# Optimization experiments

Measured on AMD Instinct MI355X. Metric: run time of the kernel, lower is better.

The kernel has to match this reference:

```python
import jax, jax.numpy as jnp
import numpy as np

TOP_K = 8
TEMPERATURE = 0.07
EPS = 1e-12  # matches torch F.normalize eps


def l2norm(x):
    return x / jnp.maximum(jnp.linalg.norm(x, axis=-1, keepdims=True), EPS)


def setup_inputs() -> dict:
    key = jax.random.key(0)
    k1, k2, k3, k4 = jax.random.split(key, 4)
    B, D, V, U, Q = 256, 768, 50257, 1000, 10000
    time_series_embedding = jax.random.normal(k1, (B, D), dtype=jnp.float32)
    word_embeddings = jax.random.normal(k2, (V, D), dtype=jnp.float32)
    # xavier_uniform-like init scale for the prototype parameter
    limit = float(np.sqrt(6.0 / (U + D)))
    tctp_embeddings = jax.random.uniform(k3, (U, D), dtype=jnp.float32, minval=-limit, maxval=limit)
    support_set = jax.random.normal(k4, (Q, D), dtype=jnp.float32)
    return {
        "time_series_embedding": time_series_embedding,
        "word_embeddings": word_embeddings,
        "tctp_embeddings": tctp_embeddings,
        "support_set": support_set,
    }


def reference(time_series_embedding, word_embeddings, tctp_embeddings, support_set):
    B = time_series_embedding.shape[0]

    # ---- L_proto: MSE between each word token and its nearest prototype ----
    # For unit vectors, cdist^2 = 2 - 2*cos_sim, so argmin(dist) == argmax(sim).
    w_norm = l2norm(word_embeddings)          # [V, D]
    t_norm = l2norm(tctp_embeddings)          # [U, D]
    sim_vu = jnp.einsum('vd,ud->vu', w_norm, t_norm)  # [V, U]
    nearest_idx = jnp.argmax(sim_vu, axis=1)          # [V]
    nearest_protos = t_norm[nearest_idx]              # [V, D]
    loss_proto = jnp.mean((w_norm - nearest_protos) ** 2)

    # ---- top-k nearest-neighbor TCTPs from the support set ----
    ts_norm = l2norm(time_series_embedding)   # [B, D]
    sup_norm = l2norm(support_set)            # [Q, D]
    sim_bq = jnp.einsum('bd,qd->bq', ts_norm, sup_norm)  # [B, Q]
    # smallest L2 distance == largest cosine similarity (unit vectors)
    _, topk_idx = jax.lax.top_k(sim_bq, TOP_K)           # [B, k]
    nearest_tctps = sup_norm[topk_idx]                   # [B, k, D]

    # ---- NNCL contrastive loss ----
    positive = l2norm(nearest_tctps.mean(axis=1))        # [B, D]
    pos_sim = jnp.sum(ts_norm * positive, axis=1) / TEMPERATURE   # [B]
    neg_sim = jnp.einsum('bd,cd->bc', ts_norm, ts_norm) / TEMPERATURE  # [B, B]
    neg_sim = jnp.where(jnp.eye(B, dtype=bool), -jnp.inf, neg_sim)
    logits = jnp.concatenate([pos_sim[:, None], neg_sim], axis=1)  # [B, 1+B]
    loss_nncl = -jnp.mean(jax.nn.log_softmax(logits, axis=1)[:, 0])

    return nearest_tctps, loss_proto, loss_nncl
```

## Files before the change

### kernel.cpp

```cpp
#include <hip/hip_runtime.h>
#include <hip/hip_bf16.h>
#include <math.h>

typedef __bf16 bf16_t;
typedef __bf16 bf16x8 __attribute__((ext_vector_type(8)));
typedef __bf16 bf16x4 __attribute__((ext_vector_type(4)));
typedef float  f32x4  __attribute__((ext_vector_type(4)));
typedef long   i64_t;
typedef unsigned long long u64_t;

#define D 768

__device__ inline double blk_sum(double x, double* s) {
#pragma unroll
  for (int m = 32; m; m >>= 1) x += __shfl_xor(x, m);
  __syncthreads();
  if ((threadIdx.x & 63) == 0) s[threadIdx.x >> 6] = x;
  __syncthreads();
  return s[0] + s[1] + s[2] + s[3];
}

__device__ inline double blk_max(double x, double* s) {
#pragma unroll
  for (int m = 32; m; m >>= 1) x = fmax(x, __shfl_xor(x, m));
  __syncthreads();
  if ((threadIdx.x & 63) == 0) s[threadIdx.x >> 6] = x;
  __syncthreads();
  return fmax(fmax(s[0], s[1]), fmax(s[2], s[3]));
}

__global__ __launch_bounds__(256) void norm_all(
    const float* __restrict__ Tm, const float* __restrict__ TS,
    const float* __restrict__ SUP, const float* __restrict__ Wm,
    u64_t* __restrict__ t8T, u64_t* __restrict__ w8t,
    float* __restrict__ wscale, float* __restrict__ ts_n,
    bf16_t* __restrict__ ts_bf, float* __restrict__ sup_n,
    double* __restrict__ accd,
    int U, int V, int B, int Q, int nbW, int nbT, int nbTS) {
  const int wave = threadIdx.x >> 6, lane = threadIdx.x & 63;
  const int bid = blockIdx.x;
  if (bid == 0 && threadIdx.x == 0) accd[0] = 0.0;

  if (bid < nbW) {
    const int v0 = bid * 64 + wave * 16;
    const int r  = lane & 15;
    const int cs = lane >> 4;
    const int v  = v0 + r;
    const bool valid = v < V;
    const float* Wp = Wm + (size_t)v * D;
    u64_t* tile = w8t + (size_t)(v0 >> 4) * 1536;
    float ssf = 0.f;
#pragma unroll
    for (int j = 0; j < 24; j++) {
      u64_t frag = 0ull;
      if (valid) {
        const float* p = Wp + (j * 4 + cs) * 8;
        float4 x = *(const float4*)p;
        float4 y = *(const float4*)(p + 4);
        ssf += x.x * x.x + x.y * x.y + x.z * x.z + x.w * x.w +
               y.x * y.x + y.y * y.y + y.z * y.z + y.w * y.w;
        int lo = __builtin_amdgcn_cvt_pk_fp8_f32(x.x * 16.f, x.y * 16.f, 0, false);
        lo = __builtin_amdgcn_cvt_pk_fp8_f32(x.z * 16.f, x.w * 16.f, lo, true);
        int hi = __builtin_amdgcn_cvt_pk_fp8_f32(y.x * 16.f, y.y * 16.f, 0, false);
        hi = __builtin_amdgcn_cvt_pk_fp8_f32(y.z * 16.f, y.w * 16.f, hi, true);
        frag = ((u64_t)(unsigned)hi << 32) | (unsigned)lo;
      }
      tile[j * 64 + lane] = frag;
    }
    ssf += __shfl_xor(ssf, 16);
    ssf += __shfl_xor(ssf, 32);
    if (cs == 0)
      wscale[v0 + r] = valid
          ? (float)(1.0 / (256.0 * fmax(sqrt((double)ssf), 1e-12)))
          : 0.f;
    return;
  }

  if (bid < nbW + nbT) {
    const int row = (bid - nbW) * 4 + wave;
    double inv = 0.0;
    if (row < U) {
      const float4* s = (const float4*)(Tm + (size_t)row * D);
      double ss = 0.0;
#pragma unroll
      for (int j = 0; j < 3; j++) {
        float4 v = s[lane + 64 * j];
        ss += (double)v.x * v.x + (double)v.y * v.y +
              (double)v.z * v.z + (double)v.w * v.w;
      }
#pragma unroll
      for (int m = 32; m; m >>= 1) ss += __shfl_xor(ss, m);
      inv = 1.0 / fmax(sqrt(ss), 1e-12);
    }
    const float sc = (float)(inv * 16.0);
#pragma unroll
    for (int h = 0; h < 2; h++) {
      if (h == 1 && lane >= 32) continue;
      const int c = h * 64 + lane;
      u64_t frag = 0ull;
      if (row < U) {
        const float* p = Tm + (size_t)row * D + c * 8;
        float4 x = *(const float4*)p;
        float4 y = *(const float4*)(p + 4);
        int lo = __builtin_amdgcn_cvt_pk_fp8_f32(x.x * sc, x.y * sc, 0, false);
        lo = __builtin_amdgcn_cvt_pk_fp8_f32(x.z * sc, x.w * sc, lo, true);
        int hi = __builtin_amdgcn_cvt_pk_fp8_f32(y.x * sc, y.y * sc, 0, false);
        hi = __builtin_amdgcn_cvt_pk_fp8_f32(y.z * sc, y.w * sc, hi, true);
        frag = ((u64_t)(unsigned)hi << 32) | (unsigned)lo;
      }
      t8T[(size_t)c * 1024 + row] = frag;
    }
    return;
  }

  const float* src;
  int row;
  bool is_ts = false;
  if (bid < nbW + nbT + nbTS) { row = (bid - nbW - nbT) * 4 + wave; src = TS; is_ts = true; }
  else                        { row = (bid - nbW - nbT - nbTS) * 4 + wave; src = SUP;
                                if (row >= Q) return; }
  const float4* s = (const float4*)(src + (size_t)row * D);
  float4 v[3];
  double ss = 0.0;
#pragma unroll
  for (int j = 0; j < 3; j++) {
    v[j] = s[lane + 64 * j];
    ss += (double)v[j].x * v[j].x + (double)v[j].y * v[j].y +
          (double)v[j].z * v[j].z + (double)v[j].w * v[j].w;
  }
#pragma unroll
  for (int m = 32; m; m >>= 1) ss += __shfl_xor(ss, m);
  double inv = 1.0 / fmax(sqrt(ss), 1e-12);
  float4 o[3];
#pragma unroll
  for (int j = 0; j < 3; j++) {
    o[j].x = (float)((double)v[j].x * inv);
    o[j].y = (float)((double)v[j].y * inv);
    o[j].z = (float)((double)v[j].z * inv);
    o[j].w = (float)((double)v[j].w * inv);
  }
  float* dst = is_ts ? ts_n : sup_n;
  float* drow = dst + (size_t)row * D;
#pragma unroll
  for (int j = 0; j < 3; j++) ((float4*)drow)[lane + 64 * j] = o[j];
  if (is_ts) {
    bf16_t* brow = ts_bf + (size_t)row * D;
#pragma unroll
    for (int j = 0; j < 3; j++) {
      bf16x4 ob;
      ob[0] = (bf16_t)o[j].x; ob[1] = (bf16_t)o[j].y;
      ob[2] = (bf16_t)o[j].z; ob[3] = (bf16_t)o[j].w;
      *(bf16x4*)(brow + 4 * (lane + 64 * j)) = ob;
    }
  }
}

__global__ __launch_bounds__(256) void maxsim_gemm(
    const u64_t* __restrict__ W8T, const u64_t* __restrict__ T8T,
    float* __restrict__ maxpart, int U, int vstride) {
  __shared__ u64_t bt[4 * 96 * 16];
  const int tid  = threadIdx.x;
  const int lane = tid & 63;
  const int r    = lane & 15;
  const int ks   = lane >> 4;
  const int g    = blockIdx.x;

  {
    const int pb = g * 64;
#pragma unroll
    for (int j = 0; j < 12; j++) {
      const int m = j * 256 + tid;
      const int s = m / 768;
      const int rem = m - s * 768;
      const int c = rem >> 3, h = rem & 7;
      ulonglong2 val = *(const ulonglong2*)(T8T + (size_t)c * 1024 + pb + s * 16 + h * 2);
      *(ulonglong2*)(bt + s * 1536 + c * 16 + h * 2) = val;
    }
  }
  __syncthreads();

  bool msk[4];
#pragma unroll
  for (int s = 0; s < 4; s++) msk[s] = (g * 64 + s * 16 + r) < U;

  const int wv = tid >> 6;
#pragma unroll
  for (int wt = 0; wt < 4; wt++) {
    const int v0 = blockIdx.y * 256 + wv * 64 + wt * 16;
    const u64_t* ap = W8T + (size_t)(v0 >> 4) * 1536;
    u64_t a[24];
#pragma unroll
    for (int kk = 0; kk < 24; kk++) a[kk] = ap[kk * 64 + lane];
    f32x4 ac0 = {0.f,0.f,0.f,0.f}, ac1 = {0.f,0.f,0.f,0.f};
    f32x4 ac2 = {0.f,0.f,0.f,0.f}, ac3 = {0.f,0.f,0.f,0.f};
#pragma unroll
    for (int kk = 0; kk < 24; kk++) {
      const int ci = kk * 64 + lane;
      ac0 = __builtin_amdgcn_mfma_f32_16x16x32_fp8_fp8(
          (i64_t)a[kk], (i64_t)bt[ci],            ac0, 0, 0, 0);
      ac1 = __builtin_amdgcn_mfma_f32_16x16x32_fp8_fp8(
          (i64_t)a[kk], (i64_t)bt[1536 + ci],     ac1, 0, 0, 0);
      ac2 = __builtin_amdgcn_mfma_f32_16x16x32_fp8_fp8(
          (i64_t)a[kk], (i64_t)bt[2 * 1536 + ci], ac2, 0, 0, 0);
      ac3 = __builtin_amdgcn_mfma_f32_16x16x32_fp8_fp8(
          (i64_t)a[kk], (i64_t)bt[3 * 1536 + ci], ac3, 0, 0, 0);
    }
    f32x4 mx = {-1e30f, -1e30f, -1e30f, -1e30f};
#pragma unroll
    for (int j = 0; j < 4; j++) {
      if (msk[0]) mx[j] = fmaxf(mx[j], ac0[j]);
      if (msk[1]) mx[j] = fmaxf(mx[j], ac1[j]);
      if (msk[2]) mx[j] = fmaxf(mx[j], ac2[j]);
      if (msk[3]) mx[j] = fmaxf(mx[j], ac3[j]);
    }
#pragma unroll
    for (int m = 1; m < 16; m <<= 1) {
#pragma unroll
      for (int j = 0; j < 4; j++) mx[j] = fmaxf(mx[j], __shfl_xor(mx[j], m));
    }
    if (r == 0) {
#pragma unroll
      for (int j = 0; j < 4; j++)
        maxpart[(size_t)g * vstride + v0 + ks * 4 + j] = mx[j];
    }
  }
}

#define LDSROW 776

__global__ __launch_bounds__(256) void simf_gemm(const float* __restrict__ SUPn,
                                                 const bf16_t* __restrict__ TSb,
                                                 float* __restrict__ sim,
                                                 int Q, int ld, int NTB) {
  __shared__ __align__(16) bf16_t lds[2][16 * LDSROW];
  const int tid  = threadIdx.x;
  const int lane = tid & 63;
  const int rowbase = blockIdx.x * 64 + (tid >> 6) * 16;
  const int arow_i  = rowbase + (lane & 15);

  bf16x8 a[24];
  if (arow_i < Q) {
    const float* ar = SUPn + (size_t)arow_i * D + ((lane >> 4) * 8);
#pragma unroll
    for (int kk = 0; kk < 24; kk++) {
      float4 x = *(const float4*)(ar + kk * 32);
      float4 y = *(const float4*)(ar + kk * 32 + 4);
      bf16x8 f;
      f[0] = (bf16_t)x.x; f[1] = (bf16_t)x.y; f[2] = (bf16_t)x.z; f[3] = (bf16_t)x.w;
      f[4] = (bf16_t)y.x; f[5] = (bf16_t)y.y; f[6] = (bf16_t)y.z; f[7] = (bf16_t)y.w;
      a[kk] = f;
    }
  } else {
#pragma unroll
    for (int kk = 0; kk < 24; kk++) {
      bf16x8 f;
#pragma unroll
      for (int e = 0; e < 8; e++) f[e] = (bf16_t)0.f;
      a[kk] = f;
    }
  }

  auto stage = [&](int buf, int nt) {
    const ulonglong2* src = (const ulonglong2*)(TSb + (size_t)nt * 16 * D);
#pragma unroll
    for (int j = 0; j < 6; j++) {
      int c = tid + j * 256;
      int rr = c / 96, w = c % 96;
      *(ulonglong2*)&lds[buf][rr * LDSROW + w * 8] = src[c];
    }
  };

  stage(0, 0);
  for (int nt = 0; nt < NTB; nt++) {
    __syncthreads();
    if (nt + 1 < NTB) stage((nt + 1) & 1, nt + 1);
    f32x4 acc = {0.f, 0.f, 0.f, 0.f};
    const bf16_t* brow = &lds[nt & 1][(lane & 15) * LDSROW + ((lane >> 4) * 8)];
#pragma unroll
    for (int kk = 0; kk < 24; kk++) {
      bf16x8 b = *(const bf16x8*)(brow + kk * 32);
      acc = __builtin_amdgcn_mfma_f32_16x16x32_bf16(a[kk], b, acc, 0, 0, 0);
    }
    const int bcol = nt * 16 + (lane & 15);
    const int q0   = rowbase + ((lane >> 4) << 2);
    float* dst = sim + (size_t)bcol * ld + q0;
    if (q0 + 3 < Q) {
      *(f32x4*)dst = acc;
    } else {
#pragma unroll
      for (int j = 0; j < 4; j++)
        if (q0 + j < Q) dst[j] = acc[j];
    }
  }
}

__device__ inline unsigned long long pack_key(float v, int q) {
  unsigned u = __float_as_uint(v);
  u = (u & 0x80000000u) ? ~u : (u | 0x80000000u);
  return ((unsigned long long)u << 32) | (unsigned)(0xFFFFFFFFu - (unsigned)q);
}

__global__ __launch_bounds__(256) void topk_nncl(const float* __restrict__ sim,
                                                 const float* __restrict__ SUPn,
                                                 const float* __restrict__ TSn,
                                                 float* __restrict__ out,
                                                 double* __restrict__ row_loss,
                                                 int Q, int ld) {
  __shared__ unsigned long long sk[256][16];
  __shared__ float tsrow[D];
  __shared__ double sval[16];
  __shared__ int    sidx[16];
  __shared__ double red[4];
  const int b = blockIdx.x, tid = threadIdx.x;
#pragma unroll
  for (int j = 0; j < 3; j++) tsrow[tid + 256 * j] = TSn[(size_t)b * D + tid + 256 * j];

  const float* row = sim + (size_t)b * ld;
  unsigned long long best[16];
#pragma unroll
  for (int k = 0; k < 16; k++) best[k] = 0ull;
  for (int q = tid; q < Q; q += 256) {
    unsigned long long key = pack_key(row[q], q);
    if (key > best[15]) {
      best[15] = key;
      for (int k = 15; k > 0; k--) {
        if (best[k] > best[k - 1]) {
          unsigned long long t = best[k]; best[k] = best[k - 1]; best[k - 1] = t;
        } else break;
      }
    }
  }
#pragma unroll
  for (int k = 0; k < 16; k++) sk[tid][k] = best[k];
  for (int stride = 128; stride >= 1; stride >>= 1) {
    __syncthreads();
    if (tid < stride) {
      unsigned long long outk[16];
      int pa = 0, pb = 0;
#pragma unroll
      for (int k = 0; k < 16; k++) {
        unsigned long long va = sk[tid][pa], vb = sk[tid + stride][pb];
        if (va >= vb) { outk[k] = va; pa++; }
        else          { outk[k] = vb; pb++; }
      }
#pragma unroll
      for (int k = 0; k < 16; k++) sk[tid][k] = outk[k];
    }
  }
  __syncthreads();

  const int lane = tid & 63, w = tid >> 6;
  for (int c = w; c < 16; c += 4) {
    int q = (int)(0xFFFFFFFFu - (unsigned)(sk[0][c] & 0xFFFFFFFFull));
    const float* sr = SUPn + (size_t)q * D;
    double dot = 0.0;
#pragma unroll
    for (int i = 0; i < 12; i++)
      dot += (double)sr[lane + 64 * i] * (double)tsrow[lane + 64 * i];
#pragma unroll
    for (int m = 32; m; m >>= 1) dot += __shfl_xor(dot, m);
    if (lane == 0) { sval[c] = dot; sidx[c] = q; }
  }
  __syncthreads();
  if (tid == 0) {
    for (int i = 1; i < 16; i++) {
      double v = sval[i]; int ix = sidx[i];
      int j = i - 1;
      while (j >= 0 && (sval[j] < v || (sval[j] == v && sidx[j] > ix))) {
        sval[j + 1] = sval[j]; sidx[j + 1] = sidx[j]; j--;
      }
      sval[j + 1] = v; sidx[j + 1] = ix;
    }
  }
  __syncthreads();

  float mean[3] = {0.f, 0.f, 0.f};
#pragma unroll
  for (int k = 0; k < 8; k++) {
    const float* sr = SUPn + (size_t)sidx[k] * D;
    float* orow = out + ((size_t)b * 8 + k) * D;
#pragma unroll
    for (int j = 0; j < 3; j++) {
      float x = sr[tid + 256 * j];
      orow[tid + 256 * j] = x;
      mean[j] += x;
    }
  }
#pragma unroll
  for (int j = 0; j < 3; j++) mean[j] *= 0.125f;
  double ss = 0.0;
#pragma unroll
  for (int j = 0; j < 3; j++) ss += (double)mean[j] * mean[j];
  ss = blk_sum(ss, red);
  double inv = 1.0 / fmax(sqrt(ss), 1e-12);
  double dot = 0.0;
#pragma unroll
  for (int j = 0; j < 3; j++)
    dot += (double)tsrow[tid + 256 * j] * ((double)mean[j] * inv);
  dot = blk_sum(dot, red);
  const double p = dot / (double)0.07f;

  const float* tc = TSn + (size_t)tid * D;
  double dot2 = 0.0;
  for (int e = 0; e < D; e += 4) {
    float4 t4 = *(const float4*)(tc + e);
    dot2 += (double)tsrow[e] * t4.x + (double)tsrow[e + 1] * t4.y +
            (double)tsrow[e + 2] * t4.z + (double)tsrow[e + 3] * t4.w;
  }
  const bool diag = (tid == b);
  double logit = dot2 / (double)0.07f;
  double m = blk_max(diag ? -1e300 : logit, red);
  m = fmax(m, p);
  double term = diag ? 0.0 : exp(logit - m);
  double ssum = blk_sum(term, red);
  ssum += exp(p - m);
  if (tid == 0) row_loss[b] = (log(ssum) + m) - p;
}

__global__ __launch_bounds__(256) void reduce_proto(
    const float* __restrict__ maxpart, const float* __restrict__ wscale,
    double* __restrict__ accd, int V, int vstride) {
  __shared__ double red[4];
  const int v = blockIdx.x * 256 + threadIdx.x;
  double s = 0.0;
  if (v < V) {
    float mx = -1e30f;
#pragma unroll
    for (int g = 0; g < 16; g++)
      mx = fmaxf(mx, maxpart[(size_t)g * vstride + v]);
    s = 2.0 - 2.0 * (double)mx * (double)wscale[v];
  }
  s = blk_sum(s, red);
  if (threadIdx.x == 0) atomicAdd(accd, s);
}

__global__ __launch_bounds__(256) void finalize(const double* __restrict__ accd,
                                                const double* __restrict__ row_loss,
                                                float* __restrict__ d_out, int out_size,
                                                int V, int B) {
  __shared__ double red[4];
  const int tid = threadIdx.x;
  double s2 = 0.0;
  for (int b = tid; b < B; b += 256) s2 += row_loss[b];
  s2 = blk_sum(s2, red);
  if (tid == 0) {
    d_out[out_size - 2] = (float)(accd[0] / ((double)V * (double)D));
    d_out[out_size - 1] = (float)(s2 / (double)B);
  }
}

extern "C" void kernel_launch(void* const* d_in, const int* in_sizes, int n_in,
                              void* d_out, int out_size, void* d_ws, size_t ws_size,
                              hipStream_t stream) {
  const float* TS  = (const float*)d_in[0];
  const float* W   = (const float*)d_in[1];
  const float* T   = (const float*)d_in[2];
  const float* SUP = (const float*)d_in[3];
  const int B = in_sizes[0] / D;
  const int V = in_sizes[1] / D;
  const int U = in_sizes[2] / D;
  const int Q = in_sizes[3] / D;
  const int VPAD = (V + 255) & ~255;
  const int QPAD = (Q + 63) & ~63;
  const int NTB  = B / 16;
  const int nbW  = VPAD / 64;
  const int nbT  = 1024 / 4;
  const int nbTS = B / 4;
  const int nbSUP = (Q + 3) / 4;

  char* ws = (char*)d_ws;
  size_t off = 0;
  auto alloc = [&](size_t bytes) -> char* {
    char* p = ws + off;
    off = (off + bytes + 255) & ~(size_t)255;
    return p;
  };
  u64_t*  t8T    = (u64_t*) alloc((size_t)96 * 1024 * 8);
  u64_t*  w8t    = (u64_t*) alloc((size_t)(VPAD / 16) * 1536 * 8);
  float*  wscale = (float*) alloc((size_t)VPAD * 4);
  float*  maxpart= (float*) alloc((size_t)16 * VPAD * 4);
  float*  ts_n   = (float*) alloc((size_t)B * D * 4);
  bf16_t* ts_bf  = (bf16_t*)alloc((size_t)B * D * 2);
  float*  sup_n  = (float*) alloc((size_t)Q * D * 4);
  float*  simf   = (float*) alloc((size_t)B * QPAD * 4);
  double* rloss  = (double*)alloc((size_t)B * 8);
  double* accd   = (double*)alloc(8);
  (void)ws_size; (void)n_in;

  norm_all<<<nbW + nbT + nbTS + nbSUP, 256, 0, stream>>>(
      T, TS, SUP, W, t8T, w8t, wscale, ts_n, ts_bf, sup_n, accd,
      U, V, B, Q, nbW, nbT, nbTS);

  dim3 gms(16, VPAD / 256);
  maxsim_gemm<<<gms, 256, 0, stream>>>(w8t, t8T, maxpart, U, VPAD);

  simf_gemm<<<QPAD / 64, 256, 0, stream>>>(sup_n, ts_bf, simf, Q, QPAD, NTB);
  topk_nncl<<<B, 256, 0, stream>>>(simf, sup_n, ts_n, (float*)d_out, rloss, Q, QPAD);
  reduce_proto<<<VPAD / 256, 256, 0, stream>>>(maxpart, wscale, accd, V, VPAD);
  finalize<<<1, 256, 0, stream>>>(accd, rloss, (float*)d_out, out_size, V, B);
}
```

Before: 212.1 us.

## Restructure top-k/NNCL kernel to 1024 threads with wave-shuffle bitonic merges

Raises the topk_nncl block to 1024 threads and replaces the shared-memory tree of sequential 16-way merges with register-level bitonic merges over wave shuffles, followed by a small cross-wave merge. The NNCL negative-similarity dot products are split four ways across thread groups and combined through shared memory. The aim is to shorten the serial merge chain and cut per-thread work in this 256-block kernel. In exchange it uses more registers per thread, and the extra shuffles may limit how many blocks run at once.

```diff
diff --git a/kernel.cpp b/kernel.cpp
--- a/kernel.cpp
+++ b/kernel.cpp
@@ -20,13 +20,28 @@
   return s[0] + s[1] + s[2] + s[3];
 }
 
-__device__ inline double blk_max(double x, double* s) {
+__device__ inline double blk_sum16(double x, double* s) {
+#pragma unroll
+  for (int m = 32; m; m >>= 1) x += __shfl_xor(x, m);
+  __syncthreads();
+  if ((threadIdx.x & 63) == 0) s[threadIdx.x >> 6] = x;
+  __syncthreads();
+  double t = 0.0;
+#pragma unroll
+  for (int i = 0; i < 16; i++) t += s[i];
+  return t;
+}
+
+__device__ inline double blk_max16(double x, double* s) {
 #pragma unroll
   for (int m = 32; m; m >>= 1) x = fmax(x, __shfl_xor(x, m));
   __syncthreads();
   if ((threadIdx.x & 63) == 0) s[threadIdx.x >> 6] = x;
   __syncthreads();
-  return fmax(fmax(s[0], s[1]), fmax(s[2], s[3]));
+  double t = s[0];
+#pragma unroll
+  for (int i = 1; i < 16; i++) t = fmax(t, s[i]);
+  return t;
 }
 
 __global__ __launch_bounds__(256) void norm_all(
@@ -300,58 +315,82 @@
   return ((unsigned long long)u << 32) | (unsigned)(0xFFFFFFFFu - (unsigned)q);
 }
 
-__global__ __launch_bounds__(256) void topk_nncl(const float* __restrict__ sim,
-                                                 const float* __restrict__ SUPn,
-                                                 const float* __restrict__ TSn,
-                                                 float* __restrict__ out,
-                                                 double* __restrict__ row_loss,
-                                                 int Q, int ld) {
-  __shared__ unsigned long long sk[256][16];
+__device__ inline void kmerge(u64_t* a, int off) {
+  u64_t m[16];
+#pragma unroll
+  for (int i = 0; i < 16; i++) {
+    u64_t o = __shfl_xor(a[15 - i], off);
+    m[i] = a[i] > o ? a[i] : o;
+  }
+#pragma unroll
+  for (int s = 8; s >= 1; s >>= 1) {
+#pragma unroll
+    for (int i = 0; i < 16; i++) {
+      if ((i & s) == 0) {
+        u64_t x = m[i], y = m[i | s];
+        m[i]     = x > y ? x : y;
+        m[i | s] = x > y ? y : x;
+      }
+    }
+  }
+#pragma unroll
+  for (int i = 0; i < 16; i++) a[i] = m[i];
+}
+
+__global__ __launch_bounds__(1024) void topk_nncl(const float* __restrict__ sim,
+                                                  const float* __restrict__ SUPn,
+                                                  const float* __restrict__ TSn,
+                                                  float* __restrict__ out,
+                                                  double* __restrict__ row_loss,
+                                                  int Q, int ld, int Bn) {
   __shared__ float tsrow[D];
+  __shared__ u64_t wk[16][16];
+  __shared__ u64_t merged[16];
   __shared__ double sval[16];
   __shared__ int    sidx[16];
-  __shared__ double red[4];
+  __shared__ double red[16];
+  __shared__ double dotbuf[4][256];
   const int b = blockIdx.x, tid = threadIdx.x;
-#pragma unroll
-  for (int j = 0; j < 3; j++) tsrow[tid + 256 * j] = TSn[(size_t)b * D + tid + 256 * j];
+  const int lane = tid & 63, wv = tid >> 6;
+  if (tid < D) tsrow[tid] = TSn[(size_t)b * D + tid];
 
   const float* row = sim + (size_t)b * ld;
-  unsigned long long best[16];
+  u64_t best[16];
 #pragma unroll
   for (int k = 0; k < 16; k++) best[k] = 0ull;
-  for (int q = tid; q < Q; q += 256) {
-    unsigned long long key = pack_key(row[q], q);
+  for (int q = tid; q < Q; q += 1024) {
+    u64_t key = pack_key(row[q], q);
     if (key > best[15]) {
       best[15] = key;
       for (int k = 15; k > 0; k--) {
         if (best[k] > best[k - 1]) {
-          unsigned long long t = best[k]; best[k] = best[k - 1]; best[k - 1] = t;
+          u64_t t = best[k]; best[k] = best[k - 1]; best[k - 1] = t;
         } else break;
       }
     }
   }
 #pragma unroll
-  for (int k = 0; k < 16; k++) sk[tid][k] = best[k];
-  for (int stride = 128; stride >= 1; stride >>= 1) {
-    __syncthreads();
-    if (tid < stride) {
-      unsigned long long outk[16];
-      int pa = 0, pb = 0;
-#pragma unroll
-      for (int k = 0; k < 16; k++) {
-        unsigned long long va = sk[tid][pa], vb = sk[tid + stride][pb];
-        if (va >= vb) { outk[k] = va; pa++; }
-        else          { outk[k] = vb; pb++; }
-      }
-#pragma unroll
-      for (int k = 0; k < 16; k++) sk[tid][k] = outk[k];
-    }
-  }
-  __syncthreads();
-
-  const int lane = tid & 63, w = tid >> 6;
-  for (int c = w; c < 16; c += 4) {
-    int q = (int)(0xFFFFFFFFu - (unsigned)(sk[0][c] & 0xFFFFFFFFull));
+  for (int off = 1; off < 64; off <<= 1) kmerge(best, off);
+  if (lane == 0) {
+#pragma unroll
+    for (int k = 0; k < 16; k++) wk[wv][k] = best[k];
+  }
+  __syncthreads();
+  if (wv == 0 && lane < 16) {
+    u64_t cur[16];
+#pragma unroll
+    for (int k = 0; k < 16; k++) cur[k] = wk[lane][k];
+#pragma unroll
+    for (int off = 1; off < 16; off <<= 1) kmerge(cur, off);
+    if (lane == 0) {
+#pragma unroll
+      for (int k = 0; k < 16; k++) merged[k] = cur[k];
+    }
+  }
+  __syncthreads();
+
+  {
+    int q = (int)(0xFFFFFFFFu - (unsigned)(merged[wv] & 0xFFFFFFFFull));
     const float* sr = SUPn + (size_t)q * D;
     double dot = 0.0;
 #pragma unroll
@@ -359,7 +398,7 @@
       dot += (double)sr[lane + 64 * i] * (double)tsrow[lane + 64 * i];
 #pragma unroll
     for (int m = 32; m; m >>= 1) dot += __shfl_xor(dot, m);
-    if (lane == 0) { sval[c] = dot; sidx[c] = q; }
+    if (lane == 0) { sval[wv] = dot; sidx[wv] = q; }
   }
   __syncthreads();
   if (tid == 0) {
@@ -374,47 +413,49 @@
   }
   __syncthreads();
 
-  float mean[3] = {0.f, 0.f, 0.f};
-#pragma unroll
-  for (int k = 0; k < 8; k++) {
-    const float* sr = SUPn + (size_t)sidx[k] * D;
-    float* orow = out + ((size_t)b * 8 + k) * D;
-#pragma unroll
-    for (int j = 0; j < 3; j++) {
-      float x = sr[tid + 256 * j];
-      orow[tid + 256 * j] = x;
-      mean[j] += x;
-    }
-  }
-#pragma unroll
-  for (int j = 0; j < 3; j++) mean[j] *= 0.125f;
-  double ss = 0.0;
-#pragma unroll
-  for (int j = 0; j < 3; j++) ss += (double)mean[j] * mean[j];
-  ss = blk_sum(ss, red);
+  float mean = 0.f;
+  if (tid < D) {
+#pragma unroll
+    for (int k = 0; k < 8; k++) {
+      float x = SUPn[(size_t)sidx[k] * D + tid];
+      out[((size_t)b * 8 + k) * D + tid] = x;
+      mean += x;
+    }
+    mean *= 0.125f;
+  }
+  double ss = blk_sum16(tid < D ? (double)mean * mean : 0.0, red);
   double inv = 1.0 / fmax(sqrt(ss), 1e-12);
-  double dot = 0.0;
-#pragma unroll
-  for (int j = 0; j < 3; j++)
-    dot += (double)tsrow[tid + 256 * j] * ((double)mean[j] * inv);
-  dot = blk_sum(dot, red);
-  const double p = dot / (double)0.07f;
-
-  const float* tc = TSn + (size_t)tid * D;
-  double dot2 = 0.0;
-  for (int e = 0; e < D; e += 4) {
-    float4 t4 = *(const float4*)(tc + e);
-    dot2 += (double)tsrow[e] * t4.x + (double)tsrow[e + 1] * t4.y +
-            (double)tsrow[e + 2] * t4.z + (double)tsrow[e + 3] * t4.w;
-  }
-  const bool diag = (tid == b);
-  double logit = dot2 / (double)0.07f;
-  double m = blk_max(diag ? -1e300 : logit, red);
+  double dotp = blk_sum16(tid < D ? (double)tsrow[tid] * ((double)mean * inv) : 0.0, red);
+  const double p = dotp / (double)0.07f;
+
+  {
+    const int c = tid & 255, pt = tid >> 8;
+    const float* tc = TSn + (size_t)c * D + pt * 192;
+    const float* tb = tsrow + pt * 192;
+    double d2 = 0.0;
+#pragma unroll
+    for (int e = 0; e < 192; e += 4) {
+      float4 t4 = *(const float4*)(tc + e);
+      d2 += (double)tb[e] * t4.x + (double)tb[e + 1] * t4.y +
+            (double)tb[e + 2] * t4.z + (double)tb[e + 3] * t4.w;
+    }
+    dotbuf[pt][c] = d2;
+  }
+  __syncthreads();
+  double logit = -1e300;
+  bool diag = false;
+  if (tid < 256) {
+    diag = (tid == b);
+    double d2 = dotbuf[0][tid] + dotbuf[1][tid] + dotbuf[2][tid] + dotbuf[3][tid];
+    logit = d2 / (double)0.07f;
+  }
+  double m = blk_max16((tid < 256 && !diag) ? logit : -1e300, red);
   m = fmax(m, p);
-  double term = diag ? 0.0 : exp(logit - m);
-  double ssum = blk_sum(term, red);
+  double term = (tid < 256 && !diag) ? exp(logit - m) : 0.0;
+  double ssum = blk_sum16(term, red);
   ssum += exp(p - m);
   if (tid == 0) row_loss[b] = (log(ssum) + m) - p;
+  (void)Bn;
 }
 
 __global__ __launch_bounds__(256) void reduce_proto(
@@ -495,7 +536,8 @@
   maxsim_gemm<<<gms, 256, 0, stream>>>(w8t, t8T, maxpart, U, VPAD);
 
   simf_gemm<<<QPAD / 64, 256, 0, stream>>>(sup_n, ts_bf, simf, Q, QPAD, NTB);
-  topk_nncl<<<B, 256, 0, stream>>>(simf, sup_n, ts_n, (float*)d_out, rloss, Q, QPAD);
+  topk_nncl<<<B, 1024, 0, stream>>>(simf, sup_n, ts_n, (float*)d_out, rloss,
+                                    Q, QPAD, B);
   reduce_proto<<<VPAD / 256, 256, 0, stream>>>(maxpart, wscale, accd, V, VPAD);
   finalize<<<1, 256, 0, stream>>>(accd, rloss, (float*)d_out, out_size, V, B);
 }
```

Measured after the change: 225.2 us. 6.2% more time.
